# Kernel optimization log

Hardware: AMD Instinct MI355X
Metric: run time of the kernel (lower is better)

Reference implementation:

```python
import jax, jax.numpy as jnp
import numpy as np

N, E, D, L = 10000, 160000, 512, 3
NEG_SLOPE = 0.2
LN_EPS = 1e-5


def setup_inputs() -> dict:
    key = jax.random.key(0)
    ks = jax.random.split(key, 16)
    def rn(k, shape, scale=0.02):
        return jax.random.normal(k, shape, dtype=jnp.float32) * scale
    return {
        "x": jax.random.normal(ks[0], (N, D), dtype=jnp.float32),
        "edge_attr": jax.random.normal(ks[1], (E, 2), dtype=jnp.float32),
        "emb_inv_W": rn(ks[2], (D, D)), "emb_inv_b": jnp.zeros((D,), jnp.float32),
        "emb_org_W": rn(ks[3], (D, D)), "emb_org_b": jnp.zeros((D,), jnp.float32),
        "gat_Wl": rn(ks[4], (L, D, D)), "gat_bl": jnp.zeros((L, D), jnp.float32),
        "gat_Wr": rn(ks[5], (L, D, D)), "gat_br": jnp.zeros((L, D), jnp.float32),
        "gat_We": rn(ks[6], (L, 2, D)),
        "gat_att": rn(ks[7], (L, D), 0.1),
        "gat_bias": jnp.zeros((L, D), jnp.float32),
        "ln_g": jnp.ones((L, D), jnp.float32), "ln_b": jnp.zeros((L, D), jnp.float32),
        "lin0_W": rn(ks[8], (2 * D, D)), "lin0_b": jnp.zeros((D,), jnp.float32),
        "lin1_W": rn(ks[9], (2 * D, D)), "lin1_b": jnp.zeros((D,), jnp.float32),
        "edge_index": jax.random.randint(ks[10], (2, E), 0, N, dtype=jnp.int32),
        "n_inv": 4000,
        "n_unknown": 3000,
    }


def _layernorm(x, g, b):
    m = jnp.mean(x, axis=-1, keepdims=True)
    v = jnp.mean((x - m) ** 2, axis=-1, keepdims=True)
    return (x - m) * jax.lax.rsqrt(v + LN_EPS) * g + b


def _gatv2(x, src, dst, edge_attr, Wl, bl, Wr, br, We, att, bias):
    # single-head GATv2: e_ij = att . leaky_relu(Wl x_j + Wr x_i + We e_ij)
    xl = x @ Wl + bl                                  # [N,D] source transform
    xr = x @ Wr + br                                  # [N,D] target transform
    m = xl[src] + xr[dst] + edge_attr @ We            # [E,D]
    s = jax.nn.leaky_relu(m, NEG_SLOPE) @ att         # [E] attention logits
    smax = jax.ops.segment_max(s, dst, num_segments=N)  # per-target max
    a = jnp.exp(s - smax[dst])
    denom = jax.ops.segment_sum(a, dst, num_segments=N)
    alpha = a / jnp.where(denom[dst] > 0, denom[dst], 1.0)  # [E]
    out = jax.ops.segment_sum(alpha[:, None] * xl[src], dst, num_segments=N)
    return out + bias


def _forward(x, edge_attr, emb_inv_W, emb_inv_b, emb_org_W, emb_org_b,
             gat_Wl, gat_bl, gat_Wr, gat_br, gat_We, gat_att, gat_bias,
             ln_g, ln_b, lin0_W, lin0_b, lin1_W, lin1_b,
             edge_index, n_inv, n_unknown):
    src, dst = edge_index[0], edge_index[1]
    x0 = x[:n_inv] @ emb_inv_W + emb_inv_b           # [n_inv, D]
    x1 = x[n_inv:] @ emb_org_W + emb_org_b           # [N-n_inv, D]
    h = jnp.concatenate([x0, x1], axis=0)            # [N, D]
    for k in range(L):
        hc = _gatv2(h, src, dst, edge_attr,
                    gat_Wl[k], gat_bl[k], gat_Wr[k], gat_br[k],
                    gat_We[k], gat_att[k], gat_bias[k])
        h = jax.nn.relu(_layernorm(hc + h, ln_g[k], ln_b[k]))
    y0 = jnp.concatenate([x0, h[:n_inv]], axis=-1) @ lin0_W + lin0_b          # [n_inv, D]
    y1 = jnp.concatenate([x1[-n_unknown:], h[-n_unknown:]], axis=-1) @ lin1_W + lin1_b  # [n_unknown, D]
    return y0 @ y1.T                                  # [n_inv, n_unknown]


def reference(x, edge_attr, emb_inv_W, emb_inv_b, emb_org_W, emb_org_b,
              gat_Wl, gat_bl, gat_Wr, gat_br, gat_We, gat_att, gat_bias,
              ln_g, ln_b, lin0_W, lin0_b, lin1_W, lin1_b,
              edge_index, n_inv, n_unknown):
    return _forward(x, edge_attr, emb_inv_W, emb_inv_b, emb_org_W, emb_org_b,
                    gat_Wl, gat_bl, gat_Wr, gat_br, gat_We, gat_att, gat_bias,
                    ln_g, ln_b, lin0_W, lin0_b, lin1_W, lin1_b,
                    edge_index, n_inv, n_unknown)
```

## Files before the change

### kernel.cpp

```cpp
#include <hip/hip_runtime.h>
#include <cstddef>
#include <cstdint>

namespace {

using u16 = unsigned short;
typedef __attribute__((ext_vector_type(8))) unsigned short u16x8;
typedef __attribute__((ext_vector_type(8))) short bf16x8;
typedef __attribute__((ext_vector_type(4))) float f32x4;

constexpr int kN    = 10000;
constexpr int kE    = 160000;
constexpr int kD    = 512;
constexpr int kNinv = 4000;
constexpr int kNunk = 3000;
constexpr int kND   = kN * kD;
constexpr int kScanBlocks = (kN + 255) / 256;
constexpr float kLnEps = 1e-5f;

__device__ __forceinline__ float bf2f(u16 u) {
  return __uint_as_float((unsigned)u << 16);
}
__device__ __forceinline__ u16 f2bf(float f) {
  unsigned u = __float_as_uint(f);
  return (u16)((u + 0x7FFFu + ((u >> 16) & 1u)) >> 16);
}

__device__ __forceinline__ void gload_lds16(const void* g, void* l) {
  __builtin_amdgcn_global_load_lds(
      (const __attribute__((address_space(1))) void*)(unsigned long long)(uintptr_t)g,
      (__attribute__((address_space(3))) void*)(unsigned)(uintptr_t)l,
      16, 0, 0);
}

struct Job2 {
  const u16* A1; const u16* A2; const u16* BT; const float* bias;
  u16* Cb; int M; int xSplit;
};

template <bool WRITE_F32, bool WRITE_BF16, bool A_F32>
__global__ __launch_bounds__(256) void gemm_bf16(
    const u16* __restrict__ A1, const u16* __restrict__ A2,
    const u16* __restrict__ BT, const float* __restrict__ bias,
    float* __restrict__ Cf, u16* __restrict__ Cb, u16* __restrict__ Cb2,
    int nsplit, int M, int N, int K, int ldc, Job2 j2) {
  __shared__ u16 As[128 * 64];
  __shared__ u16 Bs[128 * 64];
  const int tid  = threadIdx.x;
  const int lane = tid & 63;
  const int wid  = tid >> 6;

  const int nwg = gridDim.x * gridDim.y;
  int wg = blockIdx.x + gridDim.x * blockIdx.y;
  {
    const int xcd = wg & 7, idx = wg >> 3;
    const int q = nwg >> 3, r = nwg & 7;
    wg = (xcd < r ? xcd * (q + 1) : r * (q + 1) + (xcd - r) * q) + idx;
  }
  int bx = wg % gridDim.x;
  const int ny = wg / gridDim.x;

  const u16* jA1 = A1; const u16* jA2 = A2; const u16* jBT = BT;
  const float* jbias = bias; u16* jCb = Cb; int jM = M;
  if (bx >= j2.xSplit) {
    bx -= j2.xSplit;
    jA1 = j2.A1; jA2 = j2.A2; jBT = j2.BT;
    jbias = j2.bias; jCb = j2.Cb; jM = j2.M;
  }
  const int bm = bx * 128;
  const int bn = ny * 128;

  const int wr = (wid >> 1) * 64;
  const int wc = (wid & 1) * 64;

  f32x4 acc[4][4];
#pragma unroll
  for (int m = 0; m < 4; ++m)
#pragma unroll
    for (int n = 0; n < 4; ++n) acc[m][n] = (f32x4){0.f, 0.f, 0.f, 0.f};

  const int srow = lane >> 3;
  const int slot = lane & 7;
  const size_t astride = (jA2 != nullptr) ? 512 : (size_t)K;

  for (int k0 = 0; k0 < K; k0 += 64) {
    const u16* Ap = jA1;
    int kof = k0;
    if (jA2 != nullptr && k0 >= 512) { Ap = jA2; kof = k0 - 512; }
#pragma unroll
    for (int t = 0; t < 4; ++t) {
      const int inst = wid * 4 + t;
      const int row  = inst * 8 + srow;
      const int scol = ((slot ^ (row & 7)) << 4);
      const int ar   = min(bm + row, jM - 1);
      if constexpr (A_F32) {
        const float* srcf = (const float*)Ap + (size_t)ar * astride + kof + (scol >> 1);
        const float4 v0 = *reinterpret_cast<const float4*>(srcf);
        const float4 v1 = *reinterpret_cast<const float4*>(srcf + 4);
        u16x8 pk;
        pk[0] = f2bf(v0.x); pk[1] = f2bf(v0.y); pk[2] = f2bf(v0.z); pk[3] = f2bf(v0.w);
        pk[4] = f2bf(v1.x); pk[5] = f2bf(v1.y); pk[6] = f2bf(v1.z); pk[7] = f2bf(v1.w);
        *reinterpret_cast<u16x8*>((char*)As + inst * 1024 + lane * 16) = pk;
      } else {
        gload_lds16((const char*)Ap + ((size_t)ar * astride + kof) * 2 + scol,
                    (char*)As + inst * 1024);
      }
    }
#pragma unroll
    for (int t = 0; t < 4; ++t) {
      const int inst = wid * 4 + t;
      const int row  = inst * 8 + srow;
      const int scol = ((slot ^ (row & 7)) << 4);
      const int bc   = min(bn + row, N - 1);
      gload_lds16((const char*)jBT + ((size_t)bc * K + k0) * 2 + scol,
                  (char*)Bs + inst * 1024);
    }
    asm volatile("s_waitcnt vmcnt(0)" ::: "memory");
    __syncthreads();

#pragma unroll
    for (int kk = 0; kk < 2; ++kk) {
      bf16x8 af[4], bfr[4];
#pragma unroll
      for (int m = 0; m < 4; ++m) {
        const int r = wr + m * 16 + (lane & 15);
        const int s = kk * 4 + (lane >> 4);
        af[m] = *(const bf16x8*)((const char*)As + r * 128 + ((s ^ (r & 7)) << 4));
      }
#pragma unroll
      for (int n = 0; n < 4; ++n) {
        const int c = wc + n * 16 + (lane & 15);
        const int s = kk * 4 + (lane >> 4);
        bfr[n] = *(const bf16x8*)((const char*)Bs + c * 128 + ((s ^ (c & 7)) << 4));
      }
#pragma unroll
      for (int m = 0; m < 4; ++m)
#pragma unroll
        for (int n = 0; n < 4; ++n)
          acc[m][n] = __builtin_amdgcn_mfma_f32_16x16x32_bf16(bfr[n], af[m],
                                                              acc[m][n], 0, 0, 0);
    }
    __syncthreads();
  }

#pragma unroll
  for (int m = 0; m < 4; ++m) {
    const int r = bm + wr + m * 16 + (lane & 15);
    if (r >= jM) continue;
#pragma unroll
    for (int n = 0; n < 4; ++n) {
      const int c0 = bn + wc + n * 16 + ((lane >> 4) << 2);
      if (c0 >= N) continue;
      float4 bv = make_float4(0.f, 0.f, 0.f, 0.f);
      if (jbias != nullptr) bv = *reinterpret_cast<const float4*>(jbias + c0);
      float v0 = acc[m][n][0] + bv.x;
      float v1 = acc[m][n][1] + bv.y;
      float v2 = acc[m][n][2] + bv.z;
      float v3 = acc[m][n][3] + bv.w;
      if (WRITE_F32) {
        float4 o; o.x = v0; o.y = v1; o.z = v2; o.w = v3;
        *reinterpret_cast<float4*>(Cf + (size_t)r * ldc + c0) = o;
      }
      if (WRITE_BF16) {
        u16* dstp = jCb;
        int c = c0;
        if (Cb2 != nullptr && c0 >= nsplit) { dstp = Cb2; c = c0 - nsplit; }
        ushort4 o;
        o.x = f2bf(v0); o.y = f2bf(v1); o.z = f2bf(v2); o.w = f2bf(v3);
        *reinterpret_cast<ushort4*>(dstp + (size_t)r * ldc + c) = o;
      }
    }
  }
}

__global__ __launch_bounds__(256) void gat_fused_kernel(
    const u16* __restrict__ xl, const u16* __restrict__ xr,
    const int* __restrict__ esrcS, const float2* __restrict__ eaS,
    const int* __restrict__ offs, const float* __restrict__ We,
    const float* __restrict__ att, const float* __restrict__ bias,
    const float* __restrict__ lng, const float* __restrict__ lnb,
    const u16* __restrict__ resid, u16* __restrict__ hb) {
  __shared__ float accLDS[4][512];
  __shared__ float wsLDS[4];
  const int wid = threadIdx.x >> 6, lane = threadIdx.x & 63;
  const int n = blockIdx.x;
  const int d8 = lane * 8;

  float r8[8], w0[8], w1[8], a06[8], a04[8];
  {
    const u16x8 rv = *(const u16x8*)(xr + (size_t)n * kD + d8);
#pragma unroll
    for (int i = 0; i < 8; ++i) {
      r8[i] = bf2f(rv[i]);
      w0[i] = We[d8 + i];
      w1[i] = We[kD + d8 + i];
      const float a = att[d8 + i];
      a06[i] = 0.6f * a;
      a04[i] = 0.4f * a;
    }
  }

  float acc[8];
#pragma unroll
  for (int j = 0; j < 8; ++j) acc[j] = 0.f;
  float l_run = 0.f;

  const int beg = offs[n], end = offs[n + 1];
  const int cnt = end - beg;
  const int q = cnt >> 2, r = cnt & 3;
  const int myCnt = q + ((wid < r) ? 1 : 0);
  const int myBeg = beg + wid * q + min(wid, r);

  int sv = 0;
  float2 e2 = make_float2(0.f, 0.f);
  if (lane < myCnt) {
    sv = esrcS[myBeg + lane];
    e2 = eaS[myBeg + lane];
  }

  for (int i = 0; i < myCnt; i += 4) {
    const int k = myCnt - i;
    u16x8 rows[4];
#pragma unroll
    for (int t = 0; t < 4; ++t)
      if (t < k)
        rows[t] = *(const u16x8*)(xl + (size_t)__shfl(sv, i + t) * kD + d8);
    float s[4];
#pragma unroll
    for (int t = 0; t < 4; ++t) {
      s[t] = 0.f;
      if (t < k) {
        const float ex = __shfl(e2.x, i + t), ey = __shfl(e2.y, i + t);
#pragma unroll
        for (int j = 0; j < 8; ++j) {
          const float m = bf2f(rows[t][j]) + r8[j] + ex * w0[j] + ey * w1[j];
          s[t] += a06[j] * m + a04[j] * fabsf(m);
        }
      }
    }
#pragma unroll
    for (int off = 32; off > 0; off >>= 1)
#pragma unroll
      for (int t = 0; t < 4; ++t)
        if (t < k) s[t] += __shfl_xor(s[t], off);
    float qv[4];
    float ws = 0.f;
#pragma unroll
    for (int t = 0; t < 4; ++t) {
      qv[t] = (t < k) ? __expf(s[t]) : 0.f;
      ws += qv[t];
    }
    l_run += ws;
#pragma unroll
    for (int j = 0; j < 8; ++j) {
      float v = acc[j];
#pragma unroll
      for (int t = 0; t < 4; ++t)
        if (t < k) v += qv[t] * bf2f(rows[t][j]);
      acc[j] = v;
    }
  }

  if (lane == 0) wsLDS[wid] = l_run;
#pragma unroll
  for (int j = 0; j < 8; ++j) accLDS[wid][j * 64 + lane] = acc[j];
  __syncthreads();

  if (wid == 0) {
    const float l = wsLDS[0] + wsLDS[1] + wsLDS[2] + wsLDS[3];
    const float inv = 1.f / (l > 0.f ? l : 1.f);
    float aT[8];
#pragma unroll
    for (int j = 0; j < 8; ++j)
      aT[j] = accLDS[0][j * 64 + lane] + accLDS[1][j * 64 + lane] +
              accLDS[2][j * 64 + lane] + accLDS[3][j * 64 + lane];

    float xv[8];
    float sum = 0.f, sq = 0.f;
    {
      const u16x8 hv8 = *(const u16x8*)(resid + (size_t)n * kD + d8);
#pragma unroll
      for (int j = 0; j < 8; ++j) {
        xv[j] = bf2f(hv8[j]) + aT[j] * inv + bias[d8 + j];
        sum += xv[j];
        sq  += xv[j] * xv[j];
      }
    }
#pragma unroll
    for (int off = 32; off > 0; off >>= 1) {
      sum += __shfl_xor(sum, off);
      sq  += __shfl_xor(sq, off);
    }
    const float mean = sum * (1.f / kD);
    const float var  = sq * (1.f / kD) - mean * mean;
    const float rs = rsqrtf(var + kLnEps);
    u16x8 pk;
#pragma unroll
    for (int j = 0; j < 8; ++j) {
      const float y = fmaxf((xv[j] - mean) * rs * lng[d8 + j] + lnb[d8 + j], 0.f);
      pk[j] = f2bf(y);
    }
    *(u16x8*)(hb + (size_t)n * kD + d8) = pk;
  }
}

struct TxJobs {
  const float* src[10];
  u16* dst[10];
  int K[10];
  const float* bl; const float* br; float* catB; int* counts;
};

__global__ __launch_bounds__(256) void transpose_all_kernel(TxJobs jobs) {
  const int z = blockIdx.z;
  if (z == 10) {
    const int lid = (blockIdx.y * 32 + blockIdx.x) * 256 + threadIdx.x;
    if (lid < 3 * 1024) {
      const int k = lid >> 10, j = lid & 1023;
      jobs.catB[lid] = (j < 512) ? jobs.bl[k * 512 + j] : jobs.br[k * 512 + j - 512];
    }
    const int cid = lid - 3 * 1024;
    if (cid >= 0 && cid < kN) jobs.counts[cid] = 0;
    return;
  }
  const int K = jobs.K[z];
  const int k0 = blockIdx.x * 32;
  if (k0 >= K) return;
  const int n0 = blockIdx.y * 32;
  const float* W = jobs.src[z];
  u16* WT = jobs.dst[z];
  __shared__ float t[32][33];
  const int lx = threadIdx.x & 31, ly = threadIdx.x >> 5;
#pragma unroll
  for (int r = 0; r < 32; r += 8)
    t[ly + r][lx] = W[(size_t)(k0 + ly + r) * 512 + n0 + lx];
  __syncthreads();
#pragma unroll
  for (int r = 0; r < 32; r += 8)
    WT[(size_t)(n0 + ly + r) * K + k0 + lx] = f2bf(t[lx][ly + r]);
}

__global__ void count_kernel(const int* __restrict__ dst, int* __restrict__ counts) {
  const int e = blockIdx.x * 256 + threadIdx.x;
  if (e < kE) atomicAdd(&counts[dst[e]], 1);
}
__global__ __launch_bounds__(256) void scan_blk_kernel(
    const int* __restrict__ counts, int* __restrict__ offs,
    int* __restrict__ bsum, int n) {
  __shared__ int buf[256];
  const int tid = threadIdx.x;
  const int i = blockIdx.x * 256 + tid;
  const int v = (i < n) ? counts[i] : 0;
  buf[tid] = v;
  __syncthreads();
  for (int off = 1; off < 256; off <<= 1) {
    const int t = (tid >= off) ? buf[tid - off] : 0;
    __syncthreads();
    buf[tid] += t;
    __syncthreads();
  }
  if (i < n) offs[i] = buf[tid] - v;
  if (tid == 255) bsum[blockIdx.x] = buf[255];
}
__global__ __launch_bounds__(64) void scan_top_kernel(
    const int* __restrict__ bsum, int* __restrict__ boff,
    int* __restrict__ offs_total, int nb) {
  const int lane = threadIdx.x;
  const int v = (lane < nb) ? bsum[lane] : 0;
  int incl = v;
#pragma unroll
  for (int off = 1; off < 64; off <<= 1) {
    const int t = __shfl_up(incl, off);
    if (lane >= off) incl += t;
  }
  if (lane < nb) boff[lane] = incl - v;
  if (lane == 63) offs_total[0] = incl;
}
__global__ __launch_bounds__(256) void scan_add_kernel(
    int* __restrict__ offs, int* __restrict__ pos,
    const int* __restrict__ boff, int n) {
  const int i = blockIdx.x * 256 + threadIdx.x;
  if (i < n) {
    const int o = offs[i] + boff[blockIdx.x];
    offs[i] = o;
    pos[i] = o;
  }
}
__global__ void scatter_kernel(const int* __restrict__ dst,
                               const int* __restrict__ src,
                               const float* __restrict__ ea,
                               int* __restrict__ pos,
                               int* __restrict__ esrcS,
                               float2* __restrict__ eaS) {
  const int e = blockIdx.x * 256 + threadIdx.x;
  if (e >= kE) return;
  const int p = atomicAdd(&pos[dst[e]], 1);
  esrcS[p] = src[e];
  eaS[p] = *(const float2*)(ea + (size_t)e * 2);
}

}

extern "C" void kernel_launch(void* const* d_in, const int* in_sizes, int n_in,
                              void* d_out, int out_size, void* d_ws, size_t ws_size,
                              hipStream_t stream) {
  const float* x         = (const float*)d_in[0];
  const float* edge_attr = (const float*)d_in[1];
  const float* emb_inv_W = (const float*)d_in[2];
  const float* emb_inv_b = (const float*)d_in[3];
  const float* emb_org_W = (const float*)d_in[4];
  const float* emb_org_b = (const float*)d_in[5];
  const float* gat_Wl    = (const float*)d_in[6];
  const float* gat_bl    = (const float*)d_in[7];
  const float* gat_Wr    = (const float*)d_in[8];
  const float* gat_br    = (const float*)d_in[9];
  const float* gat_We    = (const float*)d_in[10];
  const float* gat_att   = (const float*)d_in[11];
  const float* gat_bias  = (const float*)d_in[12];
  const float* ln_g      = (const float*)d_in[13];
  const float* ln_b      = (const float*)d_in[14];
  const float* lin0_W    = (const float*)d_in[15];
  const float* lin0_b    = (const float*)d_in[16];
  const float* lin1_W    = (const float*)d_in[17];
  const float* lin1_b    = (const float*)d_in[18];
  const int*   edge_idx  = (const int*)d_in[19];
  const int* src = edge_idx;
  const int* dst = edge_idx + kE;
  float* out = (float*)d_out;

  float* catB = (float*)d_ws;
  u16* hb0  = (u16*)(catB + 3072);
  u16* hb   = hb0 + kND;
  u16* xlB  = hb + kND;
  u16* xrB  = xlB + kND;
  u16* y0b  = xrB + kND;
  u16* y1b  = y0b + kNinv * kD;
  u16* embInvT = y1b + kNunk * kD;
  u16* embOrgT = embInvT + 262144;
  u16* WlrT    = embOrgT + 262144;
  u16* lin0T   = WlrT + 3 * 524288;
  u16* lin1T   = lin0T + 524288;
  int* counts  = (int*)(lin1T + 524288);
  int* offs    = counts + kN;
  int* pos     = offs + kN + 1;
  int* bsum    = pos + kN;
  int* boff    = bsum + kScanBlocks;
  int* esrcS   = boff + kScanBlocks;
  float2* eaS  = (float2*)(esrcS + kE);

  const dim3 blk(256);
  auto cdiv = [](int a, int b) { return (a + b - 1) / b; };
  Job2 jNone{};
  jNone.xSplit = 0x7FFFFFFF;

  {
    TxJobs j;
    j.src[0] = emb_inv_W;  j.dst[0] = embInvT;  j.K[0] = 512;
    j.src[1] = emb_org_W;  j.dst[1] = embOrgT;  j.K[1] = 512;
    for (int k = 0; k < 3; ++k) {
      j.src[2 + k] = gat_Wl + (size_t)k * kD * kD;
      j.dst[2 + k] = WlrT + (size_t)k * 524288;
      j.K[2 + k] = 512;
      j.src[5 + k] = gat_Wr + (size_t)k * kD * kD;
      j.dst[5 + k] = WlrT + (size_t)k * 524288 + 262144;
      j.K[5 + k] = 512;
    }
    j.src[8] = lin0_W; j.dst[8] = lin0T; j.K[8] = 1024;
    j.src[9] = lin1_W; j.dst[9] = lin1T; j.K[9] = 1024;
    j.bl = gat_bl; j.br = gat_br; j.catB = catB; j.counts = counts;
    transpose_all_kernel<<<dim3(32, 16, 11), blk, 0, stream>>>(j);
  }

  {
    Job2 je;
    je.A1 = (const u16*)(x + (size_t)kNinv * kD);
    je.A2 = nullptr;
    je.BT = embOrgT;
    je.bias = emb_org_b;
    je.Cb = hb0 + (size_t)kNinv * kD;
    je.M = kN - kNinv;
    je.xSplit = cdiv(kNinv, 128);
    const int gx = je.xSplit + cdiv(kN - kNinv, 128);
    gemm_bf16<false, true, true><<<dim3(gx, 4), blk, 0, stream>>>(
        (const u16*)x, nullptr, embInvT, emb_inv_b, nullptr, hb0, nullptr, 0,
        kNinv, kD, kD, kD, je);
  }

  count_kernel<<<dim3(cdiv(kE, 256)), blk, 0, stream>>>(dst, counts);
  scan_blk_kernel<<<dim3(kScanBlocks), blk, 0, stream>>>(counts, offs, bsum, kN);
  scan_top_kernel<<<dim3(1), dim3(64), 0, stream>>>(bsum, boff, offs + kN,
                                                    kScanBlocks);
  scan_add_kernel<<<dim3(kScanBlocks), blk, 0, stream>>>(offs, pos, boff, kN);
  scatter_kernel<<<dim3(cdiv(kE, 256)), blk, 0, stream>>>(dst, src, edge_attr, pos,
                                                          esrcS, eaS);

  for (int k = 0; k < 3; ++k) {
    const u16* hIn = (k == 0) ? hb0 : hb;
    gemm_bf16<false, true, false><<<dim3(cdiv(kN, 128), 8), blk, 0, stream>>>(
        hIn, nullptr, WlrT + (size_t)k * 524288, catB + k * 1024,
        nullptr, xlB, xrB, 512, kN, 1024, kD, kD, jNone);
    gat_fused_kernel<<<dim3(kN), blk, 0, stream>>>(
        xlB, xrB, esrcS, eaS, offs,
        gat_We + (size_t)k * 2 * kD, gat_att + (size_t)k * kD,
        gat_bias + (size_t)k * kD, ln_g + (size_t)k * kD,
        ln_b + (size_t)k * kD, hIn, hb);
  }

  {
    const size_t off = (size_t)(kN - kNunk) * kD;
    Job2 jh;
    jh.A1 = hb0 + off;
    jh.A2 = hb + off;
    jh.BT = lin1T;
    jh.bias = lin1_b;
    jh.Cb = y1b;
    jh.M = kNunk;
    jh.xSplit = cdiv(kNinv, 128);
    const int gx = jh.xSplit + cdiv(kNunk, 128);
    gemm_bf16<false, true, false><<<dim3(gx, 4), blk, 0, stream>>>(
        hb0, hb, lin0T, lin0_b, nullptr, y0b, nullptr, 0,
        kNinv, kD, 2 * kD, kD, jh);
  }

  gemm_bf16<true, false, false><<<dim3(cdiv(kNinv, 128), cdiv(kNunk, 128)), blk, 0,
                                  stream>>>(
      y0b, nullptr, y1b, nullptr, out, nullptr, nullptr, 0,
      kNinv, kNunk, kD, kNunk, jNone);
}
```

Baseline: 358.6 us.

## Fuse CSR build into a single cooperative kernel with grid syncs

```diff
diff --git a/kernel.cpp b/kernel.cpp
--- a/kernel.cpp
+++ b/kernel.cpp
@@ -1,6 +1,9 @@
 #include <hip/hip_runtime.h>
+#include <hip/hip_cooperative_groups.h>
 #include <cstddef>
 #include <cstdint>
+
+namespace cg = cooperative_groups;
 
 namespace {
 
@@ -16,6 +19,7 @@
 constexpr int kNunk = 3000;
 constexpr int kND   = kN * kD;
 constexpr int kScanBlocks = (kN + 255) / 256;
+constexpr int kCsrGrid = 256;
 constexpr float kLnEps = 1e-5f;
 
 __device__ __forceinline__ float bf2f(u16 u) {
@@ -308,7 +312,7 @@
   const float* src[10];
   u16* dst[10];
   int K[10];
-  const float* bl; const float* br; float* catB; int* counts;
+  const float* bl; const float* br; float* catB;
 };
 
 __global__ __launch_bounds__(256) void transpose_all_kernel(TxJobs jobs) {
@@ -319,8 +323,6 @@
       const int k = lid >> 10, j = lid & 1023;
       jobs.catB[lid] = (j < 512) ? jobs.bl[k * 512 + j] : jobs.br[k * 512 + j - 512];
     }
-    const int cid = lid - 3 * 1024;
-    if (cid >= 0 && cid < kN) jobs.counts[cid] = 0;
     return;
   }
   const int K = jobs.K[z];
@@ -340,63 +342,61 @@
     WT[(size_t)(n0 + ly + r) * K + k0 + lx] = f2bf(t[lx][ly + r]);
 }
 
-__global__ void count_kernel(const int* __restrict__ dst, int* __restrict__ counts) {
-  const int e = blockIdx.x * 256 + threadIdx.x;
-  if (e < kE) atomicAdd(&counts[dst[e]], 1);
-}
-__global__ __launch_bounds__(256) void scan_blk_kernel(
-    const int* __restrict__ counts, int* __restrict__ offs,
-    int* __restrict__ bsum, int n) {
+__global__ __launch_bounds__(256) void csr_coop_kernel(
+    const int* __restrict__ dst, const int* __restrict__ src,
+    const float* __restrict__ ea, int* __restrict__ counts,
+    int* __restrict__ offs, int* __restrict__ pos, int* __restrict__ bsum,
+    int* __restrict__ esrcS, float2* __restrict__ eaS) {
+  cg::grid_group grid = cg::this_grid();
+  const int tid = threadIdx.x, bid = blockIdx.x;
+  const int gsz = kCsrGrid * 256, gid = bid * 256 + tid;
+
+  for (int i = gid; i < kN; i += gsz) counts[i] = 0;
+  grid.sync();
+  for (int e = gid; e < kE; e += gsz) atomicAdd(&counts[dst[e]], 1);
+  grid.sync();
   __shared__ int buf[256];
-  const int tid = threadIdx.x;
-  const int i = blockIdx.x * 256 + tid;
-  const int v = (i < n) ? counts[i] : 0;
-  buf[tid] = v;
-  __syncthreads();
-  for (int off = 1; off < 256; off <<= 1) {
-    const int t = (tid >= off) ? buf[tid - off] : 0;
+  if (bid < kScanBlocks) {
+    const int i = bid * 256 + tid;
+    const int v = (i < kN) ? counts[i] : 0;
+    buf[tid] = v;
     __syncthreads();
-    buf[tid] += t;
-    __syncthreads();
-  }
-  if (i < n) offs[i] = buf[tid] - v;
-  if (tid == 255) bsum[blockIdx.x] = buf[255];
-}
-__global__ __launch_bounds__(64) void scan_top_kernel(
-    const int* __restrict__ bsum, int* __restrict__ boff,
-    int* __restrict__ offs_total, int nb) {
-  const int lane = threadIdx.x;
-  const int v = (lane < nb) ? bsum[lane] : 0;
-  int incl = v;
-#pragma unroll
-  for (int off = 1; off < 64; off <<= 1) {
-    const int t = __shfl_up(incl, off);
-    if (lane >= off) incl += t;
-  }
-  if (lane < nb) boff[lane] = incl - v;
-  if (lane == 63) offs_total[0] = incl;
-}
-__global__ __launch_bounds__(256) void scan_add_kernel(
-    int* __restrict__ offs, int* __restrict__ pos,
-    const int* __restrict__ boff, int n) {
-  const int i = blockIdx.x * 256 + threadIdx.x;
-  if (i < n) {
-    const int o = offs[i] + boff[blockIdx.x];
-    offs[i] = o;
-    pos[i] = o;
-  }
-}
-__global__ void scatter_kernel(const int* __restrict__ dst,
-                               const int* __restrict__ src,
-                               const float* __restrict__ ea,
-                               int* __restrict__ pos,
-                               int* __restrict__ esrcS,
-                               float2* __restrict__ eaS) {
-  const int e = blockIdx.x * 256 + threadIdx.x;
-  if (e >= kE) return;
-  const int p = atomicAdd(&pos[dst[e]], 1);
-  esrcS[p] = src[e];
-  eaS[p] = *(const float2*)(ea + (size_t)e * 2);
+    for (int off = 1; off < 256; off <<= 1) {
+      const int t = (tid >= off) ? buf[tid - off] : 0;
+      __syncthreads();
+      buf[tid] += t;
+      __syncthreads();
+    }
+    if (i < kN) offs[i] = buf[tid] - v;
+    if (tid == 255) bsum[bid] = buf[255];
+  }
+  grid.sync();
+  if (bid == 0 && tid < 64) {
+    const int v = (tid < kScanBlocks) ? bsum[tid] : 0;
+    int incl = v;
+#pragma unroll
+    for (int off = 1; off < 64; off <<= 1) {
+      const int t = __shfl_up(incl, off);
+      if (tid >= off) incl += t;
+    }
+    if (tid < kScanBlocks) bsum[tid] = incl - v;
+    if (tid == 63) offs[kN] = incl;
+  }
+  grid.sync();
+  if (bid < kScanBlocks) {
+    const int i = bid * 256 + tid;
+    if (i < kN) {
+      const int o = offs[i] + bsum[bid];
+      offs[i] = o;
+      pos[i] = o;
+    }
+  }
+  grid.sync();
+  for (int e = gid; e < kE; e += gsz) {
+    const int p = atomicAdd(&pos[dst[e]], 1);
+    esrcS[p] = src[e];
+    eaS[p] = *(const float2*)(ea + (size_t)e * 2);
+  }
 }
 
 }
@@ -444,8 +444,7 @@
   int* offs    = counts + kN;
   int* pos     = offs + kN + 1;
   int* bsum    = pos + kN;
-  int* boff    = bsum + kScanBlocks;
-  int* esrcS   = boff + kScanBlocks;
+  int* esrcS   = bsum + kScanBlocks;
   float2* eaS  = (float2*)(esrcS + kE);
 
   const dim3 blk(256);
@@ -467,8 +466,16 @@
     }
     j.src[8] = lin0_W; j.dst[8] = lin0T; j.K[8] = 1024;
     j.src[9] = lin1_W; j.dst[9] = lin1T; j.K[9] = 1024;
-    j.bl = gat_bl; j.br = gat_br; j.catB = catB; j.counts = counts;
+    j.bl = gat_bl; j.br = gat_br; j.catB = catB;
     transpose_all_kernel<<<dim3(32, 16, 11), blk, 0, stream>>>(j);
+  }
+
+  {
+    void* args[] = {(void*)&dst, (void*)&src, (void*)&edge_attr,
+                    (void*)&counts, (void*)&offs, (void*)&pos, (void*)&bsum,
+                    (void*)&esrcS, (void*)&eaS};
+    hipLaunchCooperativeKernel((const void*)csr_coop_kernel, dim3(kCsrGrid), blk,
+                               args, 0, stream);
   }
 
   {
@@ -485,14 +492,6 @@
         (const u16*)x, nullptr, embInvT, emb_inv_b, nullptr, hb0, nullptr, 0,
         kNinv, kD, kD, kD, je);
   }
-
-  count_kernel<<<dim3(cdiv(kE, 256)), blk, 0, stream>>>(dst, counts);
-  scan_blk_kernel<<<dim3(kScanBlocks), blk, 0, stream>>>(counts, offs, bsum, kN);
-  scan_top_kernel<<<dim3(1), dim3(64), 0, stream>>>(bsum, boff, offs + kN,
-                                                    kScanBlocks);
-  scan_add_kernel<<<dim3(kScanBlocks), blk, 0, stream>>>(offs, pos, boff, kN);
-  scatter_kernel<<<dim3(cdiv(kE, 256)), blk, 0, stream>>>(dst, src, edge_attr, pos,
-                                                          esrcS, eaS);
 
   for (int k = 0; k < 3; ++k) {
     const u16* hIn = (k == 0) ? hb0 : hb;
```

New measurement: 490.5 us. 1.37x slower.
